# Performance work log

Hardware: AMD Instinct MI355X
Metric: run time of the kernel (lower is better)

The kernel has to match this reference:

```python
import jax, jax.numpy as jnp
import numpy as np

B, T, C = 4, 2048, 1024
H = 16
D = C // H  # head_dim = 64


def setup_inputs() -> dict:
    key = jax.random.key(0)
    k1, k2, k3, k4, k5 = jax.random.split(key, 5)
    s = 1.0 / np.sqrt(C)
    return {
        "hidden_state": jax.random.normal(k1, (B, T, C), dtype=jnp.float32),
        "qkv_w": jax.random.uniform(k2, (C, 3 * C), jnp.float32, -s, s),
        "qkv_b": jax.random.uniform(k3, (3 * C,), jnp.float32, -s, s),
        "o_w": jax.random.uniform(k4, (C, C), jnp.float32, -s, s),
        "o_b": jax.random.uniform(k5, (C,), jnp.float32, -s, s),
    }


def reference(hidden_state, qkv_w, qkv_b, o_w, o_b):
    Bq, Tq, Cq = hidden_state.shape
    qkv = hidden_state @ qkv_w + qkv_b  # [B,T,3C]
    q, k, v = jnp.split(qkv, 3, axis=-1)
    # [B,T,C] -> [B,H,T,D]
    q = q.reshape(Bq, Tq, H, D).transpose(0, 2, 1, 3)
    k = k.reshape(Bq, Tq, H, D).transpose(0, 2, 1, 3)
    v = v.reshape(Bq, Tq, H, D).transpose(0, 2, 1, 3)
    scaling = D ** (-0.5)
    scores = jnp.einsum("bhqd,bhkd->bhqk", q, k) * scaling  # [B,H,T,T]
    causal = jnp.tril(jnp.ones((Tq, Tq), dtype=bool))
    scores = jnp.where(causal[None, None], scores, -jnp.inf)
    attn = jax.nn.softmax(scores, axis=-1)
    out = jnp.einsum("bhqk,bhkd->bhqd", attn, v)  # [B,H,T,D]
    out = out.transpose(0, 2, 1, 3).reshape(Bq, Tq, Cq)
    return out @ o_w + o_b
```

## Files before the change

kernel.cpp:

```cpp
#include <hip/hip_runtime.h>
#include <hip/hip_bf16.h>

#define Bn 4
#define Tn 2048
#define Cn 1024
#define Hn 16
#define Dn 64
#define Kdim 1024

typedef __bf16 bf16x8 __attribute__((ext_vector_type(8)));
typedef float f32x4 __attribute__((ext_vector_type(4)));
union B8 { uint4 u; bf16x8 f; ushort s[8]; };

static __device__ __forceinline__ ushort f2bf(float x) {
    __hip_bfloat16 h = __float2bfloat16(x);
    return *(ushort*)&h;
}

#define AS1 __attribute__((address_space(1)))
#define AS3 __attribute__((address_space(3)))

static __device__ __forceinline__ void gload_lds16(const ushort* g, ushort* l) {
    __builtin_amdgcn_global_load_lds((AS1 const uint4*)(const void*)g,
                                     (AS3 uint4*)(void*)l, 16, 0, 0);
}

__global__ __launch_bounds__(256) void prep_fused(
    const float* __restrict__ X, const float* __restrict__ qkv_w,
    const float* __restrict__ o_w,
    ushort* __restrict__ Xb, ushort* __restrict__ Wqt, ushort* __restrict__ Wot)
{
    if (blockIdx.y == 0) {
        int i = (blockIdx.x * 256 + threadIdx.x) * 8;
        float4 a = *(const float4*)&X[i];
        float4 b = *(const float4*)&X[i + 4];
        ushort4 o0, o1;
        o0.x = f2bf(a.x); o0.y = f2bf(a.y); o0.z = f2bf(a.z); o0.w = f2bf(a.w);
        o1.x = f2bf(b.x); o1.y = f2bf(b.y); o1.z = f2bf(b.z); o1.w = f2bf(b.w);
        *(ushort4*)&Xb[i] = o0;
        *(ushort4*)&Xb[i + 4] = o1;
        return;
    }
    const float* W; ushort* Wt; int N, bx;
    if (blockIdx.y == 1) { W = qkv_w; Wt = Wqt; N = 3 * Cn; bx = blockIdx.x; }
    else                 { W = o_w;   Wt = Wot; N = Cn;     bx = blockIdx.x; }
    if (bx >= (N / 32) * 32) return;
    const int n0 = (bx % (N / 32)) * 32, k0 = (bx / (N / 32)) * 32;
    __shared__ float Ls[32][33];
    const int tx = threadIdx.x & 31, ty = threadIdx.x >> 5;
    #pragma unroll
    for (int i = 0; i < 4; i++) {
        int r = ty + i * 8;
        Ls[r][tx] = W[(size_t)(k0 + r) * N + n0 + tx];
    }
    __syncthreads();
    #pragma unroll
    for (int i = 0; i < 4; i++) {
        int r = ty + i * 8;
        Wt[(size_t)(n0 + r) * Kdim + k0 + tx] = f2bf(Ls[tx][r]);
    }
}

template <int EPI>
__global__ __launch_bounds__(256) void gemm_bt(
    const ushort* __restrict__ A, const ushort* __restrict__ Bt,
    const float* __restrict__ bias,
    float* __restrict__ Out, ushort* __restrict__ Qb,
    ushort* __restrict__ Kb, ushort* __restrict__ Vtb)
{
    const int m0 = blockIdx.y * 128;
    const int n0 = blockIdx.x * 128;
    const int t  = threadIdx.x;
    const int wave = t >> 6, lane = t & 63;
    const int ln = lane & 15, quad = lane >> 4;
    const int wm = wave >> 1, wn = wave & 1;

    __shared__ ushort As[128 * 64];
    __shared__ ushort Bs[128 * 64];

    f32x4 acc[4][4] = {};

    for (int k0 = 0; k0 < Kdim; k0 += 64) {
        __syncthreads();
        #pragma unroll
        for (int it = 0; it < 4; it++) {
            int c = it * 256 + wave * 64 + lane;
            int row = c >> 3, seg = c & 7;
            int gseg = seg ^ (row & 7);
            gload_lds16(&A [(size_t)(m0 + row) * Kdim + k0 + gseg * 8], &As[c * 8]);
            gload_lds16(&Bt[(size_t)(n0 + row) * Kdim + k0 + gseg * 8], &Bs[c * 8]);
        }
        __syncthreads();

        #pragma unroll
        for (int ks = 0; ks < 2; ks++) {
            bf16x8 af[4], bf[4];
            #pragma unroll
            for (int mm = 0; mm < 4; mm++) {
                int row = wm * 64 + mm * 16 + ln;
                int seg = (ks * 4 + quad) ^ (ln & 7);
                B8 tmp; tmp.u = *(const uint4*)&As[row * 64 + seg * 8];
                af[mm] = tmp.f;
            }
            #pragma unroll
            for (int nn = 0; nn < 4; nn++) {
                int row = wn * 64 + nn * 16 + ln;
                int seg = (ks * 4 + quad) ^ (ln & 7);
                B8 tmp; tmp.u = *(const uint4*)&Bs[row * 64 + seg * 8];
                bf[nn] = tmp.f;
            }
            #pragma unroll
            for (int mm = 0; mm < 4; mm++)
                #pragma unroll
                for (int nn = 0; nn < 4; nn++)
                    acc[mm][nn] = __builtin_amdgcn_mfma_f32_16x16x32_bf16(
                        af[mm], bf[nn], acc[mm][nn], 0, 0, 0);
        }
    }

    if (EPI == 0) {
        #pragma unroll
        for (int nn = 0; nn < 4; nn++) {
            int n = n0 + wn * 64 + nn * 16 + ln;
            float bv = bias[n];
            #pragma unroll
            for (int mm = 0; mm < 4; mm++) {
                int mbase = m0 + wm * 64 + mm * 16 + quad * 4;
                #pragma unroll
                for (int reg = 0; reg < 4; reg++)
                    Out[(size_t)(mbase + reg) * 1024 + n] = acc[mm][nn][reg] + bv;
            }
        }
    } else {
        const int nb = n0 + wn * 64;
        const int which = nb >> 10;
        const int h = (nb & 1023) >> 6;
        const float scale = (which == 0) ? 0.125f * 1.44269504088896f : 1.0f;
        const int b_ = m0 >> 11;
        const int t0 = (m0 & 2047) + wm * 64;

        __syncthreads();
        ushort* tile = ((wave & 2) ? Bs : As) + (wave & 1) * 4096;

        if (which == 2) {
            #pragma unroll
            for (int nn = 0; nn < 4; nn++) {
                float bv = bias[nb + nn * 16 + ln];
                #pragma unroll
                for (int mm = 0; mm < 4; mm++)
                    #pragma unroll
                    for (int reg = 0; reg < 4; reg++) {
                        int m = mm * 16 + quad * 4 + reg;
                        int n = nn * 16 + ln;
                        tile[n * 64 + (m ^ (((n >> 1) & 7) * 8))] =
                            f2bf(acc[mm][nn][reg] + bv);
                    }
            }
            #pragma unroll
            for (int it = 0; it < 8; it++) {
                int idx = it * 64 + lane;
                int row = idx >> 3, seg = idx & 7;
                uint4 v = *(const uint4*)&tile[row * 64 +
                              ((seg * 8) ^ (((row >> 1) & 7) * 8))];
                *(uint4*)&Vtb[((size_t)((b_ * Hn + h) * Dn) + row) * Tn + t0 + seg * 8] = v;
            }
        } else {
            ushort* dst = (which == 0) ? Qb : Kb;
            #pragma unroll
            for (int nn = 0; nn < 4; nn++) {
                float bv = bias[nb + nn * 16 + ln];
                #pragma unroll
                for (int mm = 0; mm < 4; mm++)
                    #pragma unroll
                    for (int reg = 0; reg < 4; reg++) {
                        int m = mm * 16 + quad * 4 + reg;
                        int n = nn * 16 + ln;
                        tile[m * 64 + (n ^ (((m >> 1) & 7) * 8))] =
                            f2bf((acc[mm][nn][reg] + bv) * scale);
                    }
            }
            #pragma unroll
            for (int it = 0; it < 8; it++) {
                int idx = it * 64 + lane;
                int row = idx >> 3, seg = idx & 7;
                uint4 v = *(const uint4*)&tile[row * 64 +
                              ((seg * 8) ^ (((row >> 1) & 7) * 8))];
                *(uint4*)&dst[((size_t)((b_ * Hn + h) * Tn) + t0 + row) * Dn + seg * 8] = v;
            }
        }
    }
}

__global__ __launch_bounds__(256, 2) void attn_mfma(
    const ushort* __restrict__ Qb, const ushort* __restrict__ Kb,
    const ushort* __restrict__ Vtb, ushort* __restrict__ Ob)
{
    const int bh   = blockIdx.x;
    const int yp   = blockIdx.y;
    const int t    = threadIdx.x;
    const int wave = t >> 6, lane = t & 63;
    const int ln   = lane & 15, quad = lane >> 4;

    __shared__ ushort Ks[2][128 * 64];
    __shared__ ushort Ps[4][32 * 34];

    const ushort* KgB = Kb  + (size_t)bh * Tn * Dn;
    const ushort* VgB = Vtb + (size_t)bh * Dn * Tn;
    const int b_ = bh >> 4, h = bh & 15;

    B8 ones;
    #pragma unroll
    for (int j = 0; j < 8; j++) ones.s[j] = 0x3F80;

    #define STAGE_K(kc, buf)                                                   \
        do {                                                                   \
            _Pragma("unroll")                                                  \
            for (int it = 0; it < 4; it++) {                                   \
                int c = it * 256 + wave * 64 + lane;                           \
                int row = c >> 3, seg = c & 7;                                 \
                int gs = seg ^ (row & 7);                                      \
                gload_lds16(&KgB[(size_t)((kc) * 128 + row) * Dn + gs * 8],    \
                            &Ks[buf][c * 8]);                                  \
            }                                                                  \
        } while (0)

    for (int pass = 0; pass < 2; pass++) {
        const int qt = pass ? yp : 15 - yp;
        if (pass) __syncthreads();

        int cur = 0;
        STAGE_K(0, 0);

        const int q0 = qt * 128;
        const ushort* Qg = Qb + ((size_t)bh * Tn + q0 + wave * 32) * Dn;
        bf16x8 qf[2][2];
        #pragma unroll
        for (int ns = 0; ns < 2; ns++)
            #pragma unroll
            for (int ks = 0; ks < 2; ks++) {
                B8 tmp; tmp.u = *(const uint4*)&Qg[(ns * 16 + ln) * 64 + ks * 32 + quad * 8];
                qf[ns][ks] = tmp.f;
            }

        f32x4 Oacc[4][2] = {};
        f32x4 Lacc[2] = {};
        float m_r[2] = {-1e30f, -1e30f};

        for (int kc = 0; kc <= qt; kc++) {
            __syncthreads();

            B8 vfr[4][4];
            #pragma unroll
            for (int gks = 0; gks < 4; gks++)
                #pragma unroll
                for (int ctd = 0; ctd < 4; ctd++)
                    vfr[ctd][gks].u = *(const uint4*)&VgB[
                        (size_t)(ctd * 16 + ln) * Tn + kc * 128 + gks * 32 + quad * 8];

            if (kc < qt) STAGE_K(kc + 1, cur ^ 1);

            const ushort* Kc = Ks[cur];
            f32x4 S[8][2] = {};
            #pragma unroll
            for (int ks = 0; ks < 2; ks++)
                #pragma unroll
                for (int ct = 0; ct < 8; ct++) {
                    B8 a; a.u = *(const uint4*)&Kc[(ct * 16 + ln) * 64 +
                                                   (((ks * 4 + quad) ^ (ln & 7)) * 8)];
                    #pragma unroll
                    for (int ns = 0; ns < 2; ns++)
                        S[ct][ns] = __builtin_amdgcn_mfma_f32_16x16x32_bf16(
                            a.f, qf[ns][ks], S[ct][ns], 0, 0, 0);
                }

            if (kc == qt) {
                #pragma unroll
                for (int ct = 0; ct < 8; ct++) {
                    int keyl = ct * 16 + quad * 4;
                    #pragma unroll
                    for (int ns = 0; ns < 2; ns++) {
                        int ql = wave * 32 + ns * 16 + ln;
                        #pragma unroll
                        for (int reg = 0; reg < 4; reg++)
                            if (keyl + reg > ql) S[ct][ns][reg] = -1e30f;
                    }
                }
            }

            float pmv[2];
            #pragma unroll
            for (int ns = 0; ns < 2; ns++) {
                float ctm[8];
                #pragma unroll
                for (int ct = 0; ct < 8; ct++)
                    ctm[ct] = fmaxf(fmaxf(S[ct][ns][0], S[ct][ns][1]),
                                    fmaxf(S[ct][ns][2], S[ct][ns][3]));
                float pm = fmaxf(fmaxf(fmaxf(ctm[0], ctm[1]), fmaxf(ctm[2], ctm[3])),
                                 fmaxf(fmaxf(ctm[4], ctm[5]), fmaxf(ctm[6], ctm[7])));
                pm = fmaxf(pm, __shfl_xor(pm, 16));
                pm = fmaxf(pm, __shfl_xor(pm, 32));
                pmv[ns] = pm;
            }

            bool need = (pmv[0] > m_r[0] + 8.0f) | (pmv[1] > m_r[1] + 8.0f);
            if (__any(need)) {
                #pragma unroll
                for (int ns = 0; ns < 2; ns++) {
                    float mn = fmaxf(m_r[ns], pmv[ns]);
                    float alpha = exp2f(m_r[ns] - mn);
                    m_r[ns] = mn;
                    #pragma unroll
                    for (int ctd = 0; ctd < 4; ctd++)
                        Oacc[ctd][ns] *= alpha;
                    Lacc[ns] *= alpha;
                }
            }

            ushort* Pw = Ps[wave];
            #pragma unroll
            for (int p = 0; p < 4; p++) {
                #pragma unroll
                for (int ct_h = 0; ct_h < 2; ct_h++) {
                    int ct = p * 2 + ct_h;
                    #pragma unroll
                    for (int ns = 0; ns < 2; ns++) {
                        ushort4 o;
                        #pragma unroll
                        for (int reg = 0; reg < 4; reg++) {
                            float pv = exp2f(S[ct][ns][reg] - m_r[ns]);
                            ((ushort*)&o)[reg] = f2bf(pv);
                        }
                        *(ushort4*)&Pw[(ns * 16 + ln) * 34 + ct_h * 16 + quad * 4] = o;
                    }
                }
                #pragma unroll
                for (int ns = 0; ns < 2; ns++) {
                    B8 pfr; pfr.u = *(const uint4*)&Pw[(ns * 16 + ln) * 34 + quad * 8];
                    #pragma unroll
                    for (int ctd = 0; ctd < 4; ctd++)
                        Oacc[ctd][ns] = __builtin_amdgcn_mfma_f32_16x16x32_bf16(
                            vfr[ctd][p].f, pfr.f, Oacc[ctd][ns], 0, 0, 0);
                    Lacc[ns] = __builtin_amdgcn_mfma_f32_16x16x32_bf16(
                        ones.f, pfr.f, Lacc[ns], 0, 0, 0);
                }
            }
            cur ^= 1;
        }

        #pragma unroll
        for (int ns = 0; ns < 2; ns++) {
            float inv = 1.0f / Lacc[ns][0];
            int token = q0 + wave * 32 + ns * 16 + ln;
            ushort* dst = Ob + ((size_t)(b_ * Tn + token)) * Cn + h * 64;
            #pragma unroll
            for (int ctd = 0; ctd < 4; ctd++) {
                ushort4 o;
                #pragma unroll
                for (int reg = 0; reg < 4; reg++)
                    ((ushort*)&o)[reg] = f2bf(Oacc[ctd][ns][reg] * inv);
                *(ushort4*)&dst[ctd * 16 + quad * 4] = o;
            }
        }
    }
    #undef STAGE_K
}

extern "C" void kernel_launch(void* const* d_in, const int* in_sizes, int n_in,
                              void* d_out, int out_size, void* d_ws, size_t ws_size,
                              hipStream_t stream) {
    const float* X     = (const float*)d_in[0];
    const float* qkv_w = (const float*)d_in[1];
    const float* qkv_b = (const float*)d_in[2];
    const float* o_w   = (const float*)d_in[3];
    const float* o_b   = (const float*)d_in[4];
    float* out = (float*)d_out;

    const size_t BTC = (size_t)Bn * Tn * Cn;
    ushort* Xb  = (ushort*)d_ws;
    ushort* Wqt = Xb  + BTC;
    ushort* Wot = Wqt + 3 * Cn * Cn;
    ushort* Qb  = Wot + Cn * Cn;
    ushort* Kb  = Qb  + BTC;
    ushort* Vtb = Kb  + BTC;
    ushort* Ao  = Vtb + BTC;

    prep_fused<<<dim3(4096, 3), 256, 0, stream>>>(X, qkv_w, o_w, Xb, Wqt, Wot);

    gemm_bt<1><<<dim3(3 * Cn / 128, 8192 / 128), 256, 0, stream>>>(
        Xb, Wqt, qkv_b, nullptr, Qb, Kb, Vtb);
    attn_mfma<<<dim3(Bn * Hn, 8), 256, 0, stream>>>(Qb, Kb, Vtb, Ao);
    gemm_bt<0><<<dim3(Cn / 128, 8192 / 128), 256, 0, stream>>>(
        Ao, Wot, o_b, out, nullptr, nullptr, nullptr);
}
```

Baseline: 303.4 us.

## Shrink attention query tile to 64 rows and double grid for occupancy

The attention kernel now gives each block a 64-row query tile, 16 rows per wave, instead of 128. The grid doubles to 16 blocks per head, and launch bounds go to 4 blocks per SM because register and LDS use per block shrink. The aim is more parallelism and occupancy to hide latency. In exchange, K/V loads are reused over fewer query rows, and the last key chunk of each 128-key block is partly wasted on masked keys.

```diff
diff --git a/kernel.cpp b/kernel.cpp
--- a/kernel.cpp
+++ b/kernel.cpp
@@ -191,7 +191,7 @@
     }
 }
 
-__global__ __launch_bounds__(256, 2) void attn_mfma(
+__global__ __launch_bounds__(256, 4) void attn_mfma(
     const ushort* __restrict__ Qb, const ushort* __restrict__ Kb,
     const ushort* __restrict__ Vtb, ushort* __restrict__ Ob)
 {
@@ -202,7 +202,7 @@
     const int ln   = lane & 15, quad = lane >> 4;
 
     __shared__ ushort Ks[2][128 * 64];
-    __shared__ ushort Ps[4][32 * 34];
+    __shared__ ushort Ps[4][16 * 34];
 
     const ushort* KgB = Kb  + (size_t)bh * Tn * Dn;
     const ushort* VgB = Vtb + (size_t)bh * Dn * Tn;
@@ -225,28 +225,27 @@
         } while (0)
 
     for (int pass = 0; pass < 2; pass++) {
-        const int qt = pass ? yp : 15 - yp;
+        const int j = pass ? yp : 31 - yp;
+        const int nc = (j >> 1) + 1;
         if (pass) __syncthreads();
 
         int cur = 0;
         STAGE_K(0, 0);
 
-        const int q0 = qt * 128;
-        const ushort* Qg = Qb + ((size_t)bh * Tn + q0 + wave * 32) * Dn;
-        bf16x8 qf[2][2];
+        const int q0 = j * 64;
+        const ushort* Qg = Qb + ((size_t)bh * Tn + q0 + wave * 16) * Dn;
+        bf16x8 qf[2];
         #pragma unroll
-        for (int ns = 0; ns < 2; ns++)
-            #pragma unroll
-            for (int ks = 0; ks < 2; ks++) {
-                B8 tmp; tmp.u = *(const uint4*)&Qg[(ns * 16 + ln) * 64 + ks * 32 + quad * 8];
-                qf[ns][ks] = tmp.f;
-            }
-
-        f32x4 Oacc[4][2] = {};
-        f32x4 Lacc[2] = {};
-        float m_r[2] = {-1e30f, -1e30f};
-
-        for (int kc = 0; kc <= qt; kc++) {
+        for (int ks = 0; ks < 2; ks++) {
+            B8 tmp; tmp.u = *(const uint4*)&Qg[ln * 64 + ks * 32 + quad * 8];
+            qf[ks] = tmp.f;
+        }
+
+        f32x4 Oacc[4] = {};
+        f32x4 Lacc = {};
+        float m_r = -1e30f;
+
+        for (int kc = 0; kc < nc; kc++) {
             __syncthreads();
 
             B8 vfr[4][4];
@@ -257,63 +256,49 @@
                     vfr[ctd][gks].u = *(const uint4*)&VgB[
                         (size_t)(ctd * 16 + ln) * Tn + kc * 128 + gks * 32 + quad * 8];
 
-            if (kc < qt) STAGE_K(kc + 1, cur ^ 1);
+            if (kc + 1 < nc) STAGE_K(kc + 1, cur ^ 1);
 
             const ushort* Kc = Ks[cur];
-            f32x4 S[8][2] = {};
+            f32x4 S[8] = {};
             #pragma unroll
             for (int ks = 0; ks < 2; ks++)
                 #pragma unroll
                 for (int ct = 0; ct < 8; ct++) {
                     B8 a; a.u = *(const uint4*)&Kc[(ct * 16 + ln) * 64 +
                                                    (((ks * 4 + quad) ^ (ln & 7)) * 8)];
+                    S[ct] = __builtin_amdgcn_mfma_f32_16x16x32_bf16(
+                        a.f, qf[ks], S[ct], 0, 0, 0);
+                }
+
+            if (kc == nc - 1) {
+                int ql = q0 + wave * 16 + ln;
+                #pragma unroll
+                for (int ct = 0; ct < 8; ct++) {
+                    int keyl = kc * 128 + ct * 16 + quad * 4;
                     #pragma unroll
-                    for (int ns = 0; ns < 2; ns++)
-                        S[ct][ns] = __builtin_amdgcn_mfma_f32_16x16x32_bf16(
-                            a.f, qf[ns][ks], S[ct][ns], 0, 0, 0);
+                    for (int reg = 0; reg < 4; reg++)
+                        if (keyl + reg > ql) S[ct][reg] = -1e30f;
                 }
-
-            if (kc == qt) {
-                #pragma unroll
-                for (int ct = 0; ct < 8; ct++) {
-                    int keyl = ct * 16 + quad * 4;
-                    #pragma unroll
-                    for (int ns = 0; ns < 2; ns++) {
-                        int ql = wave * 32 + ns * 16 + ln;
-                        #pragma unroll
-                        for (int reg = 0; reg < 4; reg++)
-                            if (keyl + reg > ql) S[ct][ns][reg] = -1e30f;
-                    }
-                }
-            }
-
-            float pmv[2];
-            #pragma unroll
-            for (int ns = 0; ns < 2; ns++) {
-                float ctm[8];
-                #pragma unroll
-                for (int ct = 0; ct < 8; ct++)
-                    ctm[ct] = fmaxf(fmaxf(S[ct][ns][0], S[ct][ns][1]),
-                                    fmaxf(S[ct][ns][2], S[ct][ns][3]));
-                float pm = fmaxf(fmaxf(fmaxf(ctm[0], ctm[1]), fmaxf(ctm[2], ctm[3])),
-                                 fmaxf(fmaxf(ctm[4], ctm[5]), fmaxf(ctm[6], ctm[7])));
-                pm = fmaxf(pm, __shfl_xor(pm, 16));
-                pm = fmaxf(pm, __shfl_xor(pm, 32));
-                pmv[ns] = pm;
-            }
-
-            bool need = (pmv[0] > m_r[0] + 8.0f) | (pmv[1] > m_r[1] + 8.0f);
-            if (__any(need)) {
-                #pragma unroll
-                for (int ns = 0; ns < 2; ns++) {
-                    float mn = fmaxf(m_r[ns], pmv[ns]);
-                    float alpha = exp2f(m_r[ns] - mn);
-                    m_r[ns] = mn;
-                    #pragma unroll
-                    for (int ctd = 0; ctd < 4; ctd++)
-                        Oacc[ctd][ns] *= alpha;
-                    Lacc[ns] *= alpha;
-                }
+            }
+
+            float ctm[8];
+            #pragma unroll
+            for (int ct = 0; ct < 8; ct++)
+                ctm[ct] = fmaxf(fmaxf(S[ct][0], S[ct][1]),
+                                fmaxf(S[ct][2], S[ct][3]));
+            float pm = fmaxf(fmaxf(fmaxf(ctm[0], ctm[1]), fmaxf(ctm[2], ctm[3])),
+                             fmaxf(fmaxf(ctm[4], ctm[5]), fmaxf(ctm[6], ctm[7])));
+            pm = fmaxf(pm, __shfl_xor(pm, 16));
+            pm = fmaxf(pm, __shfl_xor(pm, 32));
+
+            if (__any(pm > m_r + 8.0f)) {
+                float mn = fmaxf(m_r, pm);
+                float alpha = exp2f(m_r - mn);
+                m_r = mn;
+                #pragma unroll
+                for (int ctd = 0; ctd < 4; ctd++)
+                    Oacc[ctd] *= alpha;
+                Lacc *= alpha;
             }
 
             ushort* Pw = Ps[wave];
@@ -322,42 +307,35 @@
                 #pragma unroll
                 for (int ct_h = 0; ct_h < 2; ct_h++) {
                     int ct = p * 2 + ct_h;
+                    ushort4 o;
                     #pragma unroll
-                    for (int ns = 0; ns < 2; ns++) {
-                        ushort4 o;
-                        #pragma unroll
-                        for (int reg = 0; reg < 4; reg++) {
-                            float pv = exp2f(S[ct][ns][reg] - m_r[ns]);
-                            ((ushort*)&o)[reg] = f2bf(pv);
-                        }
-                        *(ushort4*)&Pw[(ns * 16 + ln) * 34 + ct_h * 16 + quad * 4] = o;
+                    for (int reg = 0; reg < 4; reg++) {
+                        float pv = exp2f(S[ct][reg] - m_r);
+                        ((ushort*)&o)[reg] = f2bf(pv);
                     }
+                    *(ushort4*)&Pw[ln * 34 + ct_h * 16 + quad * 4] = o;
                 }
-                #pragma unroll
-                for (int ns = 0; ns < 2; ns++) {
-                    B8 pfr; pfr.u = *(const uint4*)&Pw[(ns * 16 + ln) * 34 + quad * 8];
-                    #pragma unroll
-                    for (int ctd = 0; ctd < 4; ctd++)
-                        Oacc[ctd][ns] = __builtin_amdgcn_mfma_f32_16x16x32_bf16(
-                            vfr[ctd][p].f, pfr.f, Oacc[ctd][ns], 0, 0, 0);
-                    Lacc[ns] = __builtin_amdgcn_mfma_f32_16x16x32_bf16(
-                        ones.f, pfr.f, Lacc[ns], 0, 0, 0);
-                }
+                B8 pfr; pfr.u = *(const uint4*)&Pw[ln * 34 + quad * 8];
+                #pragma unroll
+                for (int ctd = 0; ctd < 4; ctd++)
+                    Oacc[ctd] = __builtin_amdgcn_mfma_f32_16x16x32_bf16(
+                        vfr[ctd][p].f, pfr.f, Oacc[ctd], 0, 0, 0);
+                Lacc = __builtin_amdgcn_mfma_f32_16x16x32_bf16(
+                    ones.f, pfr.f, Lacc, 0, 0, 0);
             }
             cur ^= 1;
         }
 
-        #pragma unroll
-        for (int ns = 0; ns < 2; ns++) {
-            float inv = 1.0f / Lacc[ns][0];
-            int token = q0 + wave * 32 + ns * 16 + ln;
+        {
+            float inv = 1.0f / Lacc[0];
+            int token = q0 + wave * 16 + ln;
             ushort* dst = Ob + ((size_t)(b_ * Tn + token)) * Cn + h * 64;
             #pragma unroll
             for (int ctd = 0; ctd < 4; ctd++) {
                 ushort4 o;
                 #pragma unroll
                 for (int reg = 0; reg < 4; reg++)
-                    ((ushort*)&o)[reg] = f2bf(Oacc[ctd][ns][reg] * inv);
+                    ((ushort*)&o)[reg] = f2bf(Oacc[ctd][reg] * inv);
                 *(ushort4*)&dst[ctd * 16 + quad * 4] = o;
             }
         }
@@ -388,7 +366,7 @@
 
     gemm_bt<1><<<dim3(3 * Cn / 128, 8192 / 128), 256, 0, stream>>>(
         Xb, Wqt, qkv_b, nullptr, Qb, Kb, Vtb);
-    attn_mfma<<<dim3(Bn * Hn, 8), 256, 0, stream>>>(Qb, Kb, Vtb, Ao);
+    attn_mfma<<<dim3(Bn * Hn, 16), 256, 0, stream>>>(Qb, Kb, Vtb, Ao);
     gemm_bt<0><<<dim3(Cn / 128, 8192 / 128), 256, 0, stream>>>(
         Ao, Wot, o_b, out, nullptr, nullptr, nullptr);
 }
```

Result: slower. 437.0 us (+44.0%).

## Compute softmax exponentials before rescale and batch P stores with packed bf16 conversion

Applied to the files above, without the earlier changes.

The attention kernel now exponentiates scores against the previous running max straight away. It corrects them by alpha only when a lazy rescale fires, which takes the max-reduction and rescale branch off the exp critical path. All P tiles are written into a larger per-wave LDS buffer in one pass using packed v_cvt_pk_bf16_f32, and then consumed by the PV MFMAs in a separate loop, so conversions and MFMAs are no longer interleaved. The running max now starts at 0 instead of -1e30, which relies on score magnitudes staying small enough that exp2 does not overflow. LDS use per block roughly doubles for the P buffer.

```diff
diff --git a/kernel.cpp b/kernel.cpp
--- a/kernel.cpp
+++ b/kernel.cpp
@@ -202,7 +202,7 @@
     const int ln   = lane & 15, quad = lane >> 4;
 
     __shared__ ushort Ks[2][128 * 64];
-    __shared__ ushort Ps[4][32 * 34];
+    __shared__ ushort Ps[4][2][4][16 * 34];
 
     const ushort* KgB = Kb  + (size_t)bh * Tn * Dn;
     const ushort* VgB = Vtb + (size_t)bh * Dn * Tn;
@@ -244,7 +244,7 @@
 
         f32x4 Oacc[4][2] = {};
         f32x4 Lacc[2] = {};
-        float m_r[2] = {-1e30f, -1e30f};
+        float m_r[2] = {0.f, 0.f};
 
         for (int kc = 0; kc <= qt; kc++) {
             __syncthreads();
@@ -287,28 +287,42 @@
                 }
             }
 
-            float pmv[2];
+            float pm[2], m_old[2];
             #pragma unroll
             for (int ns = 0; ns < 2; ns++) {
+                m_old[ns] = m_r[ns];
                 float ctm[8];
                 #pragma unroll
                 for (int ct = 0; ct < 8; ct++)
                     ctm[ct] = fmaxf(fmaxf(S[ct][ns][0], S[ct][ns][1]),
                                     fmaxf(S[ct][ns][2], S[ct][ns][3]));
-                float pm = fmaxf(fmaxf(fmaxf(ctm[0], ctm[1]), fmaxf(ctm[2], ctm[3])),
-                                 fmaxf(fmaxf(ctm[4], ctm[5]), fmaxf(ctm[6], ctm[7])));
-                pm = fmaxf(pm, __shfl_xor(pm, 16));
-                pm = fmaxf(pm, __shfl_xor(pm, 32));
-                pmv[ns] = pm;
-            }
-
-            bool need = (pmv[0] > m_r[0] + 8.0f) | (pmv[1] > m_r[1] + 8.0f);
+                float p = fmaxf(fmaxf(fmaxf(ctm[0], ctm[1]), fmaxf(ctm[2], ctm[3])),
+                                fmaxf(fmaxf(ctm[4], ctm[5]), fmaxf(ctm[6], ctm[7])));
+                p = fmaxf(p, __shfl_xor(p, 16));
+                p = fmaxf(p, __shfl_xor(p, 32));
+                pm[ns] = p;
+            }
+
+            #pragma unroll
+            for (int ns = 0; ns < 2; ns++)
+                #pragma unroll
+                for (int ct = 0; ct < 8; ct++)
+                    #pragma unroll
+                    for (int reg = 0; reg < 4; reg++)
+                        S[ct][ns][reg] = exp2f(S[ct][ns][reg] - m_old[ns]);
+
+            bool need = (pm[0] > m_old[0] + 8.0f) | (pm[1] > m_old[1] + 8.0f);
             if (__any(need)) {
                 #pragma unroll
                 for (int ns = 0; ns < 2; ns++) {
-                    float mn = fmaxf(m_r[ns], pmv[ns]);
-                    float alpha = exp2f(m_r[ns] - mn);
+                    float mn = fmaxf(m_old[ns], pm[ns]);
+                    float alpha = exp2f(m_old[ns] - mn);
                     m_r[ns] = mn;
+                    #pragma unroll
+                    for (int ct = 0; ct < 8; ct++)
+                        #pragma unroll
+                        for (int reg = 0; reg < 4; reg++)
+                            S[ct][ns][reg] *= alpha;
                     #pragma unroll
                     for (int ctd = 0; ctd < 4; ctd++)
                         Oacc[ctd][ns] *= alpha;
@@ -316,26 +330,26 @@
                 }
             }
 
-            ushort* Pw = Ps[wave];
-            #pragma unroll
-            for (int p = 0; p < 4; p++) {
-                #pragma unroll
-                for (int ct_h = 0; ct_h < 2; ct_h++) {
-                    int ct = p * 2 + ct_h;
-                    #pragma unroll
-                    for (int ns = 0; ns < 2; ns++) {
-                        ushort4 o;
-                        #pragma unroll
-                        for (int reg = 0; reg < 4; reg++) {
-                            float pv = exp2f(S[ct][ns][reg] - m_r[ns]);
-                            ((ushort*)&o)[reg] = f2bf(pv);
-                        }
-                        *(ushort4*)&Pw[(ns * 16 + ln) * 34 + ct_h * 16 + quad * 4] = o;
-                    }
+            #pragma unroll
+            for (int ns = 0; ns < 2; ns++)
+                #pragma unroll
+                for (int ct = 0; ct < 8; ct++) {
+                    float s0 = S[ct][ns][0], s1 = S[ct][ns][1];
+                    float s2 = S[ct][ns][2], s3 = S[ct][ns][3];
+                    uint w0, w1;
+                    asm("v_cvt_pk_bf16_f32 %0, %1, %2" : "=v"(w0) : "v"(s0), "v"(s1));
+                    asm("v_cvt_pk_bf16_f32 %0, %1, %2" : "=v"(w1) : "v"(s2), "v"(s3));
+                    uint2 o; o.x = w0; o.y = w1;
+                    *(uint2*)&Ps[wave][ns][ct >> 1]
+                        [ln * 34 + (ct & 1) * 16 + quad * 4] = o;
                 }
+
+            #pragma unroll
+            for (int p = 0; p < 4; p++)
                 #pragma unroll
                 for (int ns = 0; ns < 2; ns++) {
-                    B8 pfr; pfr.u = *(const uint4*)&Pw[(ns * 16 + ln) * 34 + quad * 8];
+                    B8 pfr; pfr.u = *(const uint4*)&Ps[wave][ns][p]
+                        [ln * 34 + quad * 8];
                     #pragma unroll
                     for (int ctd = 0; ctd < 4; ctd++)
                         Oacc[ctd][ns] = __builtin_amdgcn_mfma_f32_16x16x32_bf16(
@@ -343,7 +357,6 @@
                     Lacc[ns] = __builtin_amdgcn_mfma_f32_16x16x32_bf16(
                         ones.f, pfr.f, Lacc[ns], 0, 0, 0);
                 }
-            }
             cur ^= 1;
         }
 
```

New measurement: 271.8 us. 10.4% less time.
